# Kernel tuning notes

Measured on AMD Instinct MI355X. Metric: run time of the kernel, lower is better.

The kernel has to match this reference:

```python
import jax, jax.numpy as jnp
import numpy as np

STAGES = 3
CAUSAL = True


def sine_positional_encoding(T, D, dtype=jnp.float32):
    # keras_nlp SinePositionEncoding: interleaved sin/cos, base 10000
    pos = jnp.arange(T, dtype=dtype)[:, None]            # [T,1]
    i = jnp.arange(D)[None, :]                            # [1,D]
    angle = pos / jnp.power(jnp.asarray(10000.0, dtype), (2 * (i // 2)).astype(dtype) / D)
    return jnp.where(i % 2 == 0, jnp.sin(angle), jnp.cos(angle))  # [T,D]


def setup_inputs() -> dict:
    key = jax.random.key(0)
    kX, kWp, kbp, kWf, kbf = jax.random.split(key, 5)
    B, T, D = 4, 4096, 1024
    X = jax.random.normal(kX, (B, T, D), dtype=jnp.float32)
    # data_projection: D -> (stages+1)*D
    Wp = jax.random.normal(kWp, (D, (STAGES + 1) * D), dtype=jnp.float32) / np.sqrt(D)
    bp = jnp.zeros(((STAGES + 1) * D,), dtype=jnp.float32)
    # filters: D -> stages*D (applied to positional encoding)
    Wf = jax.random.normal(kWf, (D, STAGES * D), dtype=jnp.float32) / np.sqrt(D)
    bf = jnp.zeros((STAGES * D,), dtype=jnp.float32)
    return {"X": X, "Wp": Wp, "bp": bp, "Wf": Wf, "bf": bf}


def reference(X, Wp, bp, Wf, bf):
    B, T, D = X.shape
    # linear projections of data: [B,T,stages+1,D]
    xp = (jnp.einsum('btd,de->bte', X, Wp) + bp).reshape(B, T, STAGES + 1, D)
    # filters from sinusoidal positional encoding (batch-independent): [T,stages,D]
    pos = sine_positional_encoding(T, D, X.dtype)
    f = (pos @ Wf + bf).reshape(T, STAGES, D)
    if CAUSAL:
        # zero-pad time axis to 2T -> circular FFT conv becomes linear (causal) conv
        xp = jnp.concatenate([xp, jnp.zeros_like(xp)], axis=1)   # [B,2T,S+1,D]
        f = jnp.concatenate([f, jnp.zeros_like(f)], axis=0)      # [2T,S,D]
    L = xp.shape[1]
    F = jnp.fft.rfft(f, axis=0)                                   # [L//2+1,S,D]
    y = xp[:, :, 0, :]                                            # [B,L,D]
    for i in range(STAGES):
        conv = jnp.fft.irfft(jnp.fft.rfft(y, axis=1) * F[None, :, i, :], n=L, axis=1)
        y = conv * xp[:, :, i + 1, :]
    return y[:, :T, :] if CAUSAL else y
```

## Files before the change

kernel.cpp:

```cpp
#include <hip/hip_runtime.h>
#include <math.h>

#define T_LEN 4096
#define D_DIM 1024
#define B_DIM 4
#define N_STAGES 3
#define FT 512
#define CT 1024

typedef unsigned short bf16_t;
typedef __bf16 bf16x8 __attribute__((ext_vector_type(8)));
typedef float f32x4 __attribute__((ext_vector_type(4)));

#define PD(i) ((i) + (((unsigned)(i)) >> 3))
#define PADN 4607

__device__ __forceinline__ bf16_t f2bf(float f) {
    union { float f; unsigned u; } v; v.f = f;
    unsigned r = v.u + 0x7FFFu + ((v.u >> 16) & 1u);
    return (bf16_t)(r >> 16);
}
__device__ __forceinline__ float bf2f(bf16_t h) {
    union { unsigned u; float f; } v; v.u = ((unsigned)h) << 16;
    return v.f;
}
__device__ __forceinline__ float2 cmul(float2 a, float2 b) {
    return make_float2(a.x * b.x - a.y * b.y, a.x * b.y + a.y * b.x);
}
__device__ __forceinline__ float2 cadd(float2 a, float2 b) { return make_float2(a.x + b.x, a.y + b.y); }
__device__ __forceinline__ float2 csub(float2 a, float2 b) { return make_float2(a.x - b.x, a.y - b.y); }
__device__ __forceinline__ float2 conjf2(float2 a) { return make_float2(a.x, -a.y); }

#define GLOAD_LDS16(gp, lp) __builtin_amdgcn_global_load_lds( \
    (const __attribute__((address_space(1))) void*)(gp),      \
    (__attribute__((address_space(3))) void*)(lp), 16, 0, 0)

__global__ __launch_bounds__(256) void pos_kernel(bf16_t* __restrict__ posbf) {
    int idx = blockIdx.x * 256 + threadIdx.x;
    int t = idx >> 10;
    int k = idx & 1023;
    float e = (float)(k & ~1) / (float)D_DIM;
    float r = exp2f(-e * 13.287712379549449f);
    float angle = (float)t * r;
    float v = (k & 1) ? cosf(angle) : sinf(angle);
    posbf[idx] = f2bf(v);
}

__global__ __launch_bounds__(256) void f32_to_bf16_kernel(const float* __restrict__ in,
                                                          bf16_t* __restrict__ out, int n8) {
    int i = blockIdx.x * 256 + threadIdx.x;
    if (i >= n8) return;
    float4 a = ((const float4*)in)[i * 2];
    float4 b = ((const float4*)in)[i * 2 + 1];
    ((ushort4*)out)[i * 2]     = make_ushort4(f2bf(a.x), f2bf(a.y), f2bf(a.z), f2bf(a.w));
    ((ushort4*)out)[i * 2 + 1] = make_ushort4(f2bf(b.x), f2bf(b.y), f2bf(b.z), f2bf(b.w));
}

__global__ __launch_bounds__(256) void transpose_to_bf16(const float* __restrict__ in,
                                                         bf16_t* __restrict__ out, int K, int N) {
    __shared__ float tile[32][33];
    const int n0 = blockIdx.x * 32;
    const int k0 = blockIdx.y * 32;
    const int tx = threadIdx.x & 31;
    const int ty = threadIdx.x >> 5;
    for (int i = ty; i < 32; i += 8)
        tile[i][tx] = in[(size_t)(k0 + i) * N + n0 + tx];
    __syncthreads();
    for (int i = ty; i < 32; i += 8)
        out[(size_t)(n0 + i) * K + k0 + tx] = f2bf(tile[tx][i]);
}

template <int MODE>
__global__ __launch_bounds__(256) void mfma_gemm(const bf16_t* __restrict__ A,
                                                 const bf16_t* __restrict__ BT,
                                                 const float* __restrict__ bias,
                                                 void* __restrict__ outv,
                                                 int M, int N, int K, int nbx) {
    constexpr int SMEM_BYTES = (MODE == 0) ? (128 * 136 * 2) : (128 * 132 * 4);
    __shared__ __align__(16) char smem[SMEM_BYTES];
    bf16_t* As = (bf16_t*)smem;
    bf16_t* Bs = (bf16_t*)(smem + 8192);

    const int tid = threadIdx.x;
    const int lane = tid & 63;
    const int w = tid >> 6;
    const int wr = w >> 1, wc = w & 1;

    const int nwg = gridDim.x;
    const int q = nwg >> 3;
    const int swz = (blockIdx.x & 7) * q + (blockIdx.x >> 3);
    const int by = swz / nbx, bx = swz - by * nbx;
    const int row0 = by * 128, col0 = bx * 128;

    f32x4 acc[4][4];
#pragma unroll
    for (int m = 0; m < 4; ++m)
#pragma unroll
        for (int n = 0; n < 4; ++n) acc[m][n] = (f32x4)(0.0f);

    int offs[2], rr[2], kk8[2];
#pragma unroll
    for (int c = 0; c < 2; ++c) {
        offs[c] = (w * 2 + c) * 1024 + lane * 16;
        rr[c] = offs[c] >> 6;
        kk8[c] = ((offs[c] >> 4) & 3) * 8;
    }

    for (int k0 = 0; k0 < K; k0 += 32) {
#pragma unroll
        for (int c = 0; c < 2; ++c) {
            const bf16_t* gA = A + (size_t)(row0 + rr[c]) * K + k0 + kk8[c];
            GLOAD_LDS16(gA, As + (w * 2 + c) * 512);
            const bf16_t* gB = BT + (size_t)(col0 + rr[c]) * K + k0 + kk8[c];
            GLOAD_LDS16(gB, Bs + (w * 2 + c) * 512);
        }
        __syncthreads();

        bf16x8 af[4], bfr[4];
#pragma unroll
        for (int m = 0; m < 4; ++m)
            af[m] = *(const bf16x8*)&As[(wr * 64 + m * 16 + (lane & 15)) * 32 + (lane >> 4) * 8];
#pragma unroll
        for (int n = 0; n < 4; ++n)
            bfr[n] = *(const bf16x8*)&Bs[(wc * 64 + n * 16 + (lane & 15)) * 32 + (lane >> 4) * 8];
#pragma unroll
        for (int m = 0; m < 4; ++m)
#pragma unroll
            for (int n = 0; n < 4; ++n)
                acc[m][n] = __builtin_amdgcn_mfma_f32_16x16x32_bf16(af[m], bfr[n], acc[m][n], 0, 0, 0);
        __syncthreads();
    }

    if (MODE == 0) {
        bf16_t* Cs = (bf16_t*)smem;
#pragma unroll
        for (int m = 0; m < 4; ++m)
#pragma unroll
            for (int n = 0; n < 4; ++n) {
                int cl = wc * 64 + n * 16 + (lane & 15);
                int rlb = wr * 64 + m * 16 + ((lane >> 4) << 2);
                float bb = bias[col0 + cl];
#pragma unroll
                for (int j = 0; j < 4; ++j)
                    Cs[cl * 136 + rlb + j] = f2bf(acc[m][n][j] + bb);
            }
        __syncthreads();
        int dl = tid >> 1, th = tid & 1;
        int cc = col0 + dl;
        int s = cc >> 10, d = cc & 1023;
        int b = row0 >> 12;
        int t0 = (row0 & 4095) + th * 64;
        uint4* dst = (uint4*)&((bf16_t*)outv)[((size_t)(s * 4 + b) * 1024 + d) * 4096 + t0];
        const uint4* src = (const uint4*)&Cs[dl * 136 + th * 64];
#pragma unroll
        for (int j = 0; j < 8; ++j) dst[j] = src[j];
    } else {
        float* CsF = (float*)smem;
#pragma unroll
        for (int m = 0; m < 4; ++m)
#pragma unroll
            for (int n = 0; n < 4; ++n) {
                int cl = wc * 64 + n * 16 + (lane & 15);
                int rlb = wr * 64 + m * 16 + ((lane >> 4) << 2);
                float bb = bias[col0 + cl];
#pragma unroll
                for (int j = 0; j < 4; ++j)
                    CsF[cl * 132 + rlb + j] = acc[m][n][j] + bb;
            }
        __syncthreads();
        int dl = tid >> 1, th = tid & 1;
        int cc = col0 + dl;
        uint4* dst = (uint4*)&((float*)outv)[(size_t)cc * 4096 + row0 + th * 64];
        const uint4* src = (const uint4*)&CsF[dl * 132 + th * 64];
#pragma unroll
        for (int j = 0; j < 16; ++j) dst[j] = src[j];
    }
}

template <int INV>
__device__ __forceinline__ void bfly4(float2& a, float2& b, float2& c, float2& d) {
    float2 t0 = cadd(a, c), t1 = csub(a, c), t2 = cadd(b, d), t3 = csub(b, d);
    float2 it3 = INV ? make_float2(-t3.y, t3.x) : make_float2(t3.y, -t3.x);
    a = cadd(t0, t2); b = cadd(t1, it3); c = csub(t0, t2); d = csub(t1, it3);
}

template <int INV>
__device__ __forceinline__ void dft8(float2 (&x)[8]) {
    bfly4<INV>(x[0], x[2], x[4], x[6]);
    bfly4<INV>(x[1], x[3], x[5], x[7]);
    const float s2 = 0.70710678118654752f;
    const float2 o1 = INV ? make_float2(s2, s2) : make_float2(s2, -s2);
    const float2 o3 = INV ? make_float2(-s2, s2) : make_float2(-s2, -s2);
    x[3] = cmul(x[3], o1);
    x[5] = INV ? make_float2(-x[5].y, x[5].x) : make_float2(x[5].y, -x[5].x);
    x[7] = cmul(x[7], o3);
    float2 F0 = cadd(x[0], x[1]), F4 = csub(x[0], x[1]);
    float2 F1 = cadd(x[2], x[3]), F5 = csub(x[2], x[3]);
    float2 F2 = cadd(x[4], x[5]), F6 = csub(x[4], x[5]);
    float2 F3 = cadd(x[6], x[7]), F7 = csub(x[6], x[7]);
    x[0] = F0; x[1] = F1; x[2] = F2; x[3] = F3;
    x[4] = F4; x[5] = F5; x[6] = F6; x[7] = F7;
}

template <int INV, int M>
__device__ __forceinline__ void r8_pass(float2* __restrict__ s, const float2* __restrict__ Wu) {
    const int p = threadIdx.x;
    const int r = p & (M - 1);
    const int jm = p - r;
    float2 x[8];
#pragma unroll
    for (int c = 0; c < 8; ++c) x[c] = s[PD(p + 512 * c)];
    __syncthreads();
    dft8<INV>(x);
    const int base = 8 * jm + r;
    if (M == 512) {
#pragma unroll
        for (int q = 0; q < 8; ++q) s[PD(base + q * 512)] = x[q];
    } else {
        float2 w1 = Wu[2 * jm];
        if (INV) w1.y = -w1.y;
        float2 w2 = cmul(w1, w1);
        float2 w3 = cmul(w2, w1);
        float2 w4 = cmul(w2, w2);
        s[PD(base)]         = x[0];
        s[PD(base + M)]     = cmul(w1, x[1]);
        s[PD(base + 2 * M)] = cmul(w2, x[2]);
        s[PD(base + 3 * M)] = cmul(w3, x[3]);
        s[PD(base + 4 * M)] = cmul(w4, x[4]);
        s[PD(base + 5 * M)] = cmul(cmul(w4, w1), x[5]);
        s[PD(base + 6 * M)] = cmul(cmul(w4, w2), x[6]);
        s[PD(base + 7 * M)] = cmul(cmul(w4, w3), x[7]);
    }
    __syncthreads();
}

template <int INV>
__device__ __forceinline__ void fft4096_ip(float2* __restrict__ s, const float2* __restrict__ Wu) {
    r8_pass<INV, 1>(s, Wu);
    r8_pass<INV, 8>(s, Wu);
    r8_pass<INV, 64>(s, Wu);
    r8_pass<INV, 512>(s, Wu);
}

template <int INV, int M>
__device__ __forceinline__ void r8_pass4x(float2 (*__restrict__ s)[PADN],
                                          const float2* __restrict__ Wu) {
    const int p = threadIdx.x & 511;
    const int half = threadIdx.x >> 9;
    const int r = p & (M - 1);
    const int jm = p - r;
    const int base = 8 * jm + r;
    float2 w1, w2, w3, w4, w5, w6, w7;
    if (M != 512) {
        w1 = Wu[2 * jm];
        if (INV) w1.y = -w1.y;
        w2 = cmul(w1, w1); w3 = cmul(w2, w1); w4 = cmul(w2, w2);
        w5 = cmul(w4, w1); w6 = cmul(w4, w2); w7 = cmul(w4, w3);
    }
    float2 x[8];
#pragma unroll
    for (int c = 0; c < 8; ++c) x[c] = s[half][PD(p + 512 * c)];
    __syncthreads();
    dft8<INV>(x);
    if (M == 512) {
#pragma unroll
        for (int q = 0; q < 8; ++q) s[half][PD(base + q * 512)] = x[q];
    } else {
        s[half][PD(base)]         = x[0];
        s[half][PD(base + M)]     = cmul(w1, x[1]);
        s[half][PD(base + 2 * M)] = cmul(w2, x[2]);
        s[half][PD(base + 3 * M)] = cmul(w3, x[3]);
        s[half][PD(base + 4 * M)] = cmul(w4, x[4]);
        s[half][PD(base + 5 * M)] = cmul(w5, x[5]);
        s[half][PD(base + 6 * M)] = cmul(w6, x[6]);
        s[half][PD(base + 7 * M)] = cmul(w7, x[7]);
    }
    float2 y[8];
#pragma unroll
    for (int c = 0; c < 8; ++c) y[c] = s[2 + half][PD(p + 512 * c)];
    __syncthreads();
    dft8<INV>(y);
    if (M == 512) {
#pragma unroll
        for (int q = 0; q < 8; ++q) s[2 + half][PD(base + q * 512)] = y[q];
    } else {
        s[2 + half][PD(base)]         = y[0];
        s[2 + half][PD(base + M)]     = cmul(w1, y[1]);
        s[2 + half][PD(base + 2 * M)] = cmul(w2, y[2]);
        s[2 + half][PD(base + 3 * M)] = cmul(w3, y[3]);
        s[2 + half][PD(base + 4 * M)] = cmul(w4, y[4]);
        s[2 + half][PD(base + 5 * M)] = cmul(w5, y[5]);
        s[2 + half][PD(base + 6 * M)] = cmul(w6, y[6]);
        s[2 + half][PD(base + 7 * M)] = cmul(w7, y[7]);
    }
    __syncthreads();
}

template <int INV>
__device__ __forceinline__ void fft4096_ip4x(float2 (*__restrict__ s)[PADN],
                                             const float2* __restrict__ Wu) {
    r8_pass4x<INV, 1>(s, Wu);
    r8_pass4x<INV, 8>(s, Wu);
    r8_pass4x<INV, 64>(s, Wu);
    r8_pass4x<INV, 512>(s, Wu);
}

template <int NTHR>
__device__ __forceinline__ void init_wu(float2* __restrict__ Wu) {
    const int tid = threadIdx.x;
#pragma unroll
    for (int u = 0; u < 2048 / NTHR; ++u) {
        int k = u * NTHR + tid;
        float sn, cs;
        __sincosf((float)k * -7.669903939428206e-4f, &sn, &cs);
        Wu[k] = make_float2(cs, sn);
    }
}

__device__ __forceinline__ float2 spec_load(const void* spec, int bf, size_t row, int k) {
    if (bf) {
        ushort2 h = ((const ushort2*)spec)[row * 4097 + k];
        return make_float2(bf2f(h.x), bf2f(h.y));
    }
    return ((const float2*)spec)[row * 4097 + k];
}
__device__ __forceinline__ void spec_store(void* spec, int bf, size_t row, int k, float2 v) {
    if (bf) ((ushort2*)spec)[row * 4097 + k] = make_ushort2(f2bf(v.x), f2bf(v.y));
    else    ((float2*)spec)[row * 4097 + k] = v;
}

__global__ __launch_bounds__(FT)
void filter_fft_kernel(const float* __restrict__ fT,
                       void* __restrict__ specv,
                       int spec_bf16) {
    __shared__ __align__(16) float2 sA[PADN];
    __shared__ __align__(16) float2 Wu[2048];
    const int tid = threadIdx.x;
    const size_t row = blockIdx.x;
    init_wu<FT>(Wu);
    const float4* f4 = (const float4*)&fT[row * T_LEN];
#pragma unroll
    for (int u = 0; u < 2; ++u) {
        int j = u * FT + tid;
        float4 v = f4[j];
        sA[PD(2 * j)]     = make_float2(v.x, v.y);
        sA[PD(2 * j + 1)] = make_float2(v.z, v.w);
    }
#pragma unroll
    for (int u = 0; u < 4; ++u) {
        int n = 2048 + u * FT + tid;
        sA[PD(n)] = make_float2(0.0f, 0.0f);
    }
    __syncthreads();
    fft4096_ip<0>(sA, Wu);
#pragma unroll
    for (int u = 0; u < 4; ++u) {
        int s = u * FT + tid;
        if (s < 2047) {
            int k = s + 1, nk = 4096 - k;
            float2 Zk = sA[PD(k)], Zn = sA[PD(nk)];
            float2 Ye = make_float2(0.5f * (Zk.x + Zn.x), 0.5f * (Zk.y - Zn.y));
            float2 Yo = make_float2(0.5f * (Zk.y + Zn.y), -0.5f * (Zk.x - Zn.x));
            float2 w = Wu[k];
            float2 wYo = cmul(w, Yo);
            spec_store(specv, spec_bf16, row, k, cadd(Ye, wYo));
            spec_store(specv, spec_bf16, row, nk, conjf2(csub(Ye, wYo)));
        }
    }
    if (tid == 0) {
        float2 Z0 = sA[PD(0)];
        spec_store(specv, spec_bf16, row, 0,    make_float2(Z0.x + Z0.y, 0.0f));
        spec_store(specv, spec_bf16, row, 4096, make_float2(Z0.x - Z0.y, 0.0f));
        spec_store(specv, spec_bf16, row, 2048, conjf2(sA[PD(2048)]));
    }
}

__global__ __launch_bounds__(CT)
void conv_kernel(const bf16_t* __restrict__ xpT,
                 const void* __restrict__ specv,
                 int spec_bf16,
                 bf16_t* __restrict__ yT) {
    __shared__ __align__(16) float2 sA[4][PADN];
    __shared__ __align__(16) float2 Wu[2048];
    const int tid = threadIdx.x;
    const int d = blockIdx.x;
    init_wu<CT>(Wu);

#pragma unroll
    for (int bb = 0; bb < 4; ++bb) {
        const ushort4* y4 = (const ushort4*)&xpT[((size_t)bb * 1024 + d) * T_LEN];
        {
            int j = tid;
            ushort4 h = y4[j];
            sA[bb][PD(2 * j)]     = make_float2(bf2f(h.x), bf2f(h.y));
            sA[bb][PD(2 * j + 1)] = make_float2(bf2f(h.z), bf2f(h.w));
        }
#pragma unroll
        for (int u = 0; u < 2; ++u) {
            int n = 2048 + u * CT + tid;
            sA[bb][PD(n)] = make_float2(0.0f, 0.0f);
        }
    }
    __syncthreads();

    const float scale = 1.0f / 4096.0f;
    for (int st = 0; st < N_STAGES; ++st) {
        fft4096_ip4x<0>(sA, Wu);
        const size_t row = (size_t)st * 1024 + d;
#pragma unroll
        for (int u = 0; u < 2; ++u) {
            int s = u * CT + tid;
            if (s < 2047) {
                int k = s + 1, nk = 4096 - k;
                float2 w = Wu[k];
                float2 cw = conjf2(w);
                float2 Fk = spec_load(specv, spec_bf16, row, k);
                float2 Fn = spec_load(specv, spec_bf16, row, nk);
#pragma unroll
                for (int bb = 0; bb < 4; ++bb) {
                    float2 Zk = sA[bb][PD(k)], Zn = sA[bb][PD(nk)];
                    float2 Ye = make_float2(0.5f * (Zk.x + Zn.x), 0.5f * (Zk.y - Zn.y));
                    float2 Yo = make_float2(0.5f * (Zk.y + Zn.y), -0.5f * (Zk.x - Zn.x));
                    float2 wYo = cmul(w, Yo);
                    float2 Yk = cadd(Ye, wYo);
                    float2 Ynk = conjf2(csub(Ye, wYo));
                    float2 Hk = cmul(Yk, Fk);
                    float2 Hn = cmul(Ynk, Fn);
                    float2 He = make_float2(0.5f * (Hk.x + Hn.x), 0.5f * (Hk.y - Hn.y));
                    float2 Hd = make_float2(0.5f * (Hk.x - Hn.x), 0.5f * (Hk.y + Hn.y));
                    float2 Ho = cmul(cw, Hd);
                    sA[bb][PD(k)]  = make_float2(He.x - Ho.y, He.y + Ho.x);
                    sA[bb][PD(nk)] = make_float2(He.x + Ho.y, Ho.x - He.y);
                }
            }
        }
        if (tid == 0) {
            float2 F0 = spec_load(specv, spec_bf16, row, 0);
            float2 FN = spec_load(specv, spec_bf16, row, 4096);
            float2 F2 = spec_load(specv, spec_bf16, row, 2048);
#pragma unroll
            for (int bb = 0; bb < 4; ++bb) {
                float2 Z0 = sA[bb][PD(0)];
                float Y0 = Z0.x + Z0.y, YN = Z0.x - Z0.y;
                float2 H0 = make_float2(Y0 * F0.x, Y0 * F0.y);
                float2 HN = make_float2(YN * FN.x, YN * FN.y);
                float2 He0 = make_float2(0.5f * (H0.x + HN.x), 0.5f * (H0.y + HN.y));
                float2 Ho0 = make_float2(0.5f * (H0.x - HN.x), 0.5f * (H0.y - HN.y));
                sA[bb][PD(0)] = make_float2(He0.x - Ho0.y, He0.y + Ho0.x);
                float2 H2 = cmul(conjf2(sA[bb][PD(2048)]), F2);
                sA[bb][PD(2048)] = conjf2(H2);
            }
        }
        __syncthreads();
        fft4096_ip4x<1>(sA, Wu);

        if (st < N_STAGES - 1) {
#pragma unroll
            for (int bb = 0; bb < 4; ++bb) {
                const ushort4* g4 = (const ushort4*)&xpT[((size_t)((st + 1) * 4 + bb) * 1024 + d) * T_LEN];
                {
                    int j = tid;
                    ushort4 h = g4[j];
                    float2 v0 = sA[bb][PD(2 * j)], v1 = sA[bb][PD(2 * j + 1)];
                    sA[bb][PD(2 * j)]     = make_float2(v0.x * scale * bf2f(h.x), v0.y * scale * bf2f(h.y));
                    sA[bb][PD(2 * j + 1)] = make_float2(v1.x * scale * bf2f(h.z), v1.y * scale * bf2f(h.w));
                }
#pragma unroll
                for (int u = 0; u < 2; ++u) {
                    int n = 2048 + u * CT + tid;
                    sA[bb][PD(n)] = make_float2(0.0f, 0.0f);
                }
            }
            __syncthreads();
        } else {
#pragma unroll
            for (int bb = 0; bb < 4; ++bb) {
                const ushort4* g4 = (const ushort4*)&xpT[((size_t)((st + 1) * 4 + bb) * 1024 + d) * T_LEN];
                ushort4* yrow = (ushort4*)&yT[((size_t)bb * 1024 + d) * T_LEN];
                int j = tid;
                ushort4 h = g4[j];
                float2 v0 = sA[bb][PD(2 * j)], v1 = sA[bb][PD(2 * j + 1)];
                yrow[j] = make_ushort4(f2bf(v0.x * scale * bf2f(h.x)),
                                       f2bf(v0.y * scale * bf2f(h.y)),
                                       f2bf(v1.x * scale * bf2f(h.z)),
                                       f2bf(v1.y * scale * bf2f(h.w)));
            }
        }
    }
}

__global__ __launch_bounds__(256) void transpose_out(const bf16_t* __restrict__ yT,
                                                     float* __restrict__ out) {
    __shared__ float tile[32][33];
    const int tb = blockIdx.z;
    const int t0 = blockIdx.x * 32;
    const int d0 = blockIdx.y * 32;
    const int tx = threadIdx.x & 31;
    const int ty = threadIdx.x >> 5;
    for (int i = ty; i < 32; i += 8)
        tile[i][tx] = bf2f(yT[((size_t)tb * 1024 + d0 + i) * 4096 + t0 + tx]);
    __syncthreads();
    for (int i = ty; i < 32; i += 8)
        out[((size_t)tb * 4096 + t0 + i) * 1024 + d0 + tx] = tile[tx][i];
}

extern "C" void kernel_launch(void* const* d_in, const int* in_sizes, int n_in,
                              void* d_out, int out_size, void* d_ws, size_t ws_size,
                              hipStream_t stream) {
    const float* X   = (const float*)d_in[0];
    const float* Wp  = (const float*)d_in[1];
    const float* bp  = (const float*)d_in[2];
    const float* Wf  = (const float*)d_in[3];
    const float* bfv = (const float*)d_in[4];
    float* out = (float*)d_out;
    char* ws = (char*)d_ws;

    const size_t XPT_BYTES  = (size_t)134217728;
    const size_t SPEC_F32_B = (size_t)3 * 1024 * 4097 * 8;
    const size_t SPEC_BF_B  = (size_t)3 * 1024 * 4097 * 4;
    const size_t XBF_BYTES  = (size_t)33554432;
    const size_t WPT_BYTES  = (size_t)8388608;

    bf16_t* xpT   = (bf16_t*)ws;
    bf16_t* posbf = (bf16_t*)ws;
    bf16_t* WfT   = (bf16_t*)(ws + 16777216);
    float*  fT    = (float*)(ws + 33554432);
    void*   spec  = (void*)(ws + XPT_BYTES);

    int spec_bf16;
    size_t spec_bytes;
    if (ws_size >= XPT_BYTES + SPEC_F32_B + XBF_BYTES + WPT_BYTES) {
        spec_bf16 = 0; spec_bytes = SPEC_F32_B;
    } else {
        spec_bf16 = 1; spec_bytes = SPEC_BF_B;
    }
    bf16_t* Xbf = (bf16_t*)(ws + XPT_BYTES + spec_bytes);
    bf16_t* WpT = (bf16_t*)(ws + XPT_BYTES + spec_bytes + XBF_BYTES);
    bf16_t* yT  = Xbf;

    pos_kernel<<<(T_LEN * D_DIM) / 256, 256, 0, stream>>>(posbf);

    transpose_to_bf16<<<dim3(3072 / 32, 1024 / 32), 256, 0, stream>>>(Wf, WfT, 1024, 3072);
    mfma_gemm<1><<<768, 256, 0, stream>>>(posbf, WfT, bfv, fT, 4096, 3072, 1024, 24);

    filter_fft_kernel<<<N_STAGES * D_DIM, FT, 0, stream>>>(fT, spec, spec_bf16);

    f32_to_bf16_kernel<<<8192, 256, 0, stream>>>(X, Xbf, 2097152);
    transpose_to_bf16<<<dim3(4096 / 32, 1024 / 32), 256, 0, stream>>>(Wp, WpT, 1024, 4096);
    mfma_gemm<0><<<4096, 256, 0, stream>>>(Xbf, WpT, bp, xpT, 16384, 4096, 1024, 32);

    conv_kernel<<<D_DIM, CT, 0, stream>>>(xpT, spec, spec_bf16, yT);

    transpose_out<<<dim3(4096 / 32, 1024 / 32, B_DIM), 256, 0, stream>>>(yT, out);
}
```

Before: 721.8 us.

## Run conv kernel with 512 threads, each processing two FFT rows per pass

The conv kernel goes from 1024 to 512 threads per block. Each thread now runs the radix-8 butterflies for two batch rows at once instead of one, and all load and store loops are doubled to match. The end-of-pass barrier is removed from each radix pass, leaving a single barrier at the end of each FFT. The aim is fewer barriers and more independent work per thread. The cost is higher register pressure and half as many resident waves to hide LDS latency.

```diff
diff --git a/kernel.cpp b/kernel.cpp
--- a/kernel.cpp
+++ b/kernel.cpp
@@ -6,7 +6,6 @@
 #define B_DIM 4
 #define N_STAGES 3
 #define FT 512
-#define CT 1024
 
 typedef unsigned short bf16_t;
 typedef __bf16 bf16x8 __attribute__((ext_vector_type(8)));
@@ -243,10 +242,9 @@
 }
 
 template <int INV, int M>
-__device__ __forceinline__ void r8_pass4x(float2 (*__restrict__ s)[PADN],
+__device__ __forceinline__ void r8_pass4s(float2 (*__restrict__ s)[PADN],
                                           const float2* __restrict__ Wu) {
-    const int p = threadIdx.x & 511;
-    const int half = threadIdx.x >> 9;
+    const int p = threadIdx.x;
     const int r = p & (M - 1);
     const int jm = p - r;
     const int base = 8 * jm + r;
@@ -257,60 +255,73 @@
         w2 = cmul(w1, w1); w3 = cmul(w2, w1); w4 = cmul(w2, w2);
         w5 = cmul(w4, w1); w6 = cmul(w4, w2); w7 = cmul(w4, w3);
     }
-    float2 x[8];
-#pragma unroll
-    for (int c = 0; c < 8; ++c) x[c] = s[half][PD(p + 512 * c)];
-    __syncthreads();
-    dft8<INV>(x);
-    if (M == 512) {
-#pragma unroll
-        for (int q = 0; q < 8; ++q) s[half][PD(base + q * 512)] = x[q];
-    } else {
-        s[half][PD(base)]         = x[0];
-        s[half][PD(base + M)]     = cmul(w1, x[1]);
-        s[half][PD(base + 2 * M)] = cmul(w2, x[2]);
-        s[half][PD(base + 3 * M)] = cmul(w3, x[3]);
-        s[half][PD(base + 4 * M)] = cmul(w4, x[4]);
-        s[half][PD(base + 5 * M)] = cmul(w5, x[5]);
-        s[half][PD(base + 6 * M)] = cmul(w6, x[6]);
-        s[half][PD(base + 7 * M)] = cmul(w7, x[7]);
-    }
-    float2 y[8];
-#pragma unroll
-    for (int c = 0; c < 8; ++c) y[c] = s[2 + half][PD(p + 512 * c)];
-    __syncthreads();
-    dft8<INV>(y);
-    if (M == 512) {
-#pragma unroll
-        for (int q = 0; q < 8; ++q) s[2 + half][PD(base + q * 512)] = y[q];
-    } else {
-        s[2 + half][PD(base)]         = y[0];
-        s[2 + half][PD(base + M)]     = cmul(w1, y[1]);
-        s[2 + half][PD(base + 2 * M)] = cmul(w2, y[2]);
-        s[2 + half][PD(base + 3 * M)] = cmul(w3, y[3]);
-        s[2 + half][PD(base + 4 * M)] = cmul(w4, y[4]);
-        s[2 + half][PD(base + 5 * M)] = cmul(w5, y[5]);
-        s[2 + half][PD(base + 6 * M)] = cmul(w6, y[6]);
-        s[2 + half][PD(base + 7 * M)] = cmul(w7, y[7]);
-    }
-    __syncthreads();
+    {
+        float2 x[2][8];
+#pragma unroll
+        for (int e = 0; e < 2; ++e)
+#pragma unroll
+            for (int c = 0; c < 8; ++c) x[e][c] = s[e][PD(p + 512 * c)];
+        __syncthreads();
+#pragma unroll
+        for (int e = 0; e < 2; ++e) {
+            dft8<INV>(x[e]);
+            if (M == 512) {
+#pragma unroll
+                for (int q = 0; q < 8; ++q) s[e][PD(base + q * 512)] = x[e][q];
+            } else {
+                s[e][PD(base)]         = x[e][0];
+                s[e][PD(base + M)]     = cmul(w1, x[e][1]);
+                s[e][PD(base + 2 * M)] = cmul(w2, x[e][2]);
+                s[e][PD(base + 3 * M)] = cmul(w3, x[e][3]);
+                s[e][PD(base + 4 * M)] = cmul(w4, x[e][4]);
+                s[e][PD(base + 5 * M)] = cmul(w5, x[e][5]);
+                s[e][PD(base + 6 * M)] = cmul(w6, x[e][6]);
+                s[e][PD(base + 7 * M)] = cmul(w7, x[e][7]);
+            }
+        }
+    }
+    {
+        float2 y[2][8];
+#pragma unroll
+        for (int e = 0; e < 2; ++e)
+#pragma unroll
+            for (int c = 0; c < 8; ++c) y[e][c] = s[2 + e][PD(p + 512 * c)];
+        __syncthreads();
+#pragma unroll
+        for (int e = 0; e < 2; ++e) {
+            dft8<INV>(y[e]);
+            if (M == 512) {
+#pragma unroll
+                for (int q = 0; q < 8; ++q) s[2 + e][PD(base + q * 512)] = y[e][q];
+            } else {
+                s[2 + e][PD(base)]         = y[e][0];
+                s[2 + e][PD(base + M)]     = cmul(w1, y[e][1]);
+                s[2 + e][PD(base + 2 * M)] = cmul(w2, y[e][2]);
+                s[2 + e][PD(base + 3 * M)] = cmul(w3, y[e][3]);
+                s[2 + e][PD(base + 4 * M)] = cmul(w4, y[e][4]);
+                s[2 + e][PD(base + 5 * M)] = cmul(w5, y[e][5]);
+                s[2 + e][PD(base + 6 * M)] = cmul(w6, y[e][6]);
+                s[2 + e][PD(base + 7 * M)] = cmul(w7, y[e][7]);
+            }
+        }
+    }
 }
 
 template <int INV>
-__device__ __forceinline__ void fft4096_ip4x(float2 (*__restrict__ s)[PADN],
+__device__ __forceinline__ void fft4096_ip4s(float2 (*__restrict__ s)[PADN],
                                              const float2* __restrict__ Wu) {
-    r8_pass4x<INV, 1>(s, Wu);
-    r8_pass4x<INV, 8>(s, Wu);
-    r8_pass4x<INV, 64>(s, Wu);
-    r8_pass4x<INV, 512>(s, Wu);
-}
-
-template <int NTHR>
+    r8_pass4s<INV, 1>(s, Wu);
+    r8_pass4s<INV, 8>(s, Wu);
+    r8_pass4s<INV, 64>(s, Wu);
+    r8_pass4s<INV, 512>(s, Wu);
+    __syncthreads();
+}
+
 __device__ __forceinline__ void init_wu(float2* __restrict__ Wu) {
     const int tid = threadIdx.x;
 #pragma unroll
-    for (int u = 0; u < 2048 / NTHR; ++u) {
-        int k = u * NTHR + tid;
+    for (int u = 0; u < 4; ++u) {
+        int k = u * FT + tid;
         float sn, cs;
         __sincosf((float)k * -7.669903939428206e-4f, &sn, &cs);
         Wu[k] = make_float2(cs, sn);
@@ -337,7 +348,7 @@
     __shared__ __align__(16) float2 Wu[2048];
     const int tid = threadIdx.x;
     const size_t row = blockIdx.x;
-    init_wu<FT>(Wu);
+    init_wu(Wu);
     const float4* f4 = (const float4*)&fT[row * T_LEN];
 #pragma unroll
     for (int u = 0; u < 2; ++u) {
@@ -375,7 +386,7 @@
     }
 }
 
-__global__ __launch_bounds__(CT)
+__global__ __launch_bounds__(FT)
 void conv_kernel(const bf16_t* __restrict__ xpT,
                  const void* __restrict__ specv,
                  int spec_bf16,
@@ -384,20 +395,21 @@
     __shared__ __align__(16) float2 Wu[2048];
     const int tid = threadIdx.x;
     const int d = blockIdx.x;
-    init_wu<CT>(Wu);
+    init_wu(Wu);
 
 #pragma unroll
     for (int bb = 0; bb < 4; ++bb) {
         const ushort4* y4 = (const ushort4*)&xpT[((size_t)bb * 1024 + d) * T_LEN];
-        {
-            int j = tid;
+#pragma unroll
+        for (int u = 0; u < 2; ++u) {
+            int j = u * FT + tid;
             ushort4 h = y4[j];
             sA[bb][PD(2 * j)]     = make_float2(bf2f(h.x), bf2f(h.y));
             sA[bb][PD(2 * j + 1)] = make_float2(bf2f(h.z), bf2f(h.w));
         }
 #pragma unroll
-        for (int u = 0; u < 2; ++u) {
-            int n = 2048 + u * CT + tid;
+        for (int u = 0; u < 4; ++u) {
+            int n = 2048 + u * FT + tid;
             sA[bb][PD(n)] = make_float2(0.0f, 0.0f);
         }
     }
@@ -405,11 +417,11 @@
 
     const float scale = 1.0f / 4096.0f;
     for (int st = 0; st < N_STAGES; ++st) {
-        fft4096_ip4x<0>(sA, Wu);
+        fft4096_ip4s<0>(sA, Wu);
         const size_t row = (size_t)st * 1024 + d;
 #pragma unroll
-        for (int u = 0; u < 2; ++u) {
-            int s = u * CT + tid;
+        for (int u = 0; u < 4; ++u) {
+            int s = u * FT + tid;
             if (s < 2047) {
                 int k = s + 1, nk = 4096 - k;
                 float2 w = Wu[k];
@@ -452,22 +464,23 @@
             }
         }
         __syncthreads();
-        fft4096_ip4x<1>(sA, Wu);
+        fft4096_ip4s<1>(sA, Wu);
 
         if (st < N_STAGES - 1) {
 #pragma unroll
             for (int bb = 0; bb < 4; ++bb) {
                 const ushort4* g4 = (const ushort4*)&xpT[((size_t)((st + 1) * 4 + bb) * 1024 + d) * T_LEN];
-                {
-                    int j = tid;
+#pragma unroll
+                for (int u = 0; u < 2; ++u) {
+                    int j = u * FT + tid;
                     ushort4 h = g4[j];
                     float2 v0 = sA[bb][PD(2 * j)], v1 = sA[bb][PD(2 * j + 1)];
                     sA[bb][PD(2 * j)]     = make_float2(v0.x * scale * bf2f(h.x), v0.y * scale * bf2f(h.y));
                     sA[bb][PD(2 * j + 1)] = make_float2(v1.x * scale * bf2f(h.z), v1.y * scale * bf2f(h.w));
                 }
 #pragma unroll
-                for (int u = 0; u < 2; ++u) {
-                    int n = 2048 + u * CT + tid;
+                for (int u = 0; u < 4; ++u) {
+                    int n = 2048 + u * FT + tid;
                     sA[bb][PD(n)] = make_float2(0.0f, 0.0f);
                 }
             }
@@ -477,13 +490,16 @@
             for (int bb = 0; bb < 4; ++bb) {
                 const ushort4* g4 = (const ushort4*)&xpT[((size_t)((st + 1) * 4 + bb) * 1024 + d) * T_LEN];
                 ushort4* yrow = (ushort4*)&yT[((size_t)bb * 1024 + d) * T_LEN];
-                int j = tid;
-                ushort4 h = g4[j];
-                float2 v0 = sA[bb][PD(2 * j)], v1 = sA[bb][PD(2 * j + 1)];
-                yrow[j] = make_ushort4(f2bf(v0.x * scale * bf2f(h.x)),
-                                       f2bf(v0.y * scale * bf2f(h.y)),
-                                       f2bf(v1.x * scale * bf2f(h.z)),
-                                       f2bf(v1.y * scale * bf2f(h.w)));
+#pragma unroll
+                for (int u = 0; u < 2; ++u) {
+                    int j = u * FT + tid;
+                    ushort4 h = g4[j];
+                    float2 v0 = sA[bb][PD(2 * j)], v1 = sA[bb][PD(2 * j + 1)];
+                    yrow[j] = make_ushort4(f2bf(v0.x * scale * bf2f(h.x)),
+                                           f2bf(v0.y * scale * bf2f(h.y)),
+                                           f2bf(v1.x * scale * bf2f(h.z)),
+                                           f2bf(v1.y * scale * bf2f(h.w)));
+                }
             }
         }
     }
@@ -549,7 +565,7 @@
     transpose_to_bf16<<<dim3(4096 / 32, 1024 / 32), 256, 0, stream>>>(Wp, WpT, 1024, 4096);
     mfma_gemm<0><<<4096, 256, 0, stream>>>(Xbf, WpT, bp, xpT, 16384, 4096, 1024, 32);
 
-    conv_kernel<<<D_DIM, CT, 0, stream>>>(xpT, spec, spec_bf16, yT);
+    conv_kernel<<<D_DIM, FT, 0, stream>>>(xpT, spec, spec_bf16, yT);
 
     transpose_out<<<dim3(4096 / 32, 1024 / 32, B_DIM), 256, 0, stream>>>(yT, out);
 }
```

New measurement: 672.6 us. 6.8% less time.
